# Performance work log

Measured on AMD Instinct MI355X. Metric: run time of the kernel, lower is better.

The kernel has to match this reference:

```python
import jax, jax.numpy as jnp
import numpy as np

BATCH, SEQ, D_IN, D_OUT, RANK = 2, 4096, 4096, 4096, 16


def setup_inputs() -> dict:
    key = jax.random.key(0)
    ks = jax.random.split(key, 5)
    x = jax.random.normal(ks[0], (BATCH, SEQ, D_IN), dtype=jnp.float32)
    W = jax.random.normal(ks[1], (D_OUT, D_IN), dtype=jnp.float32) * 0.02
    bias = jax.random.normal(ks[2], (D_OUT,), dtype=jnp.float32) * 0.02
    A = jax.random.normal(ks[3], (RANK, D_IN), dtype=jnp.float32) * 0.02
    B = jax.random.normal(ks[4], (D_OUT, RANK), dtype=jnp.float32) * 0.02
    return {"x": x, "W": W, "bias": bias, "A": A, "B": B}


def reference(x, W, bias, A, B):
    # base GEMM: F.linear(x, W, bias) -> [b, s, d_out]
    base_out = jnp.einsum("bsi,oi->bso", x, W) + bias
    # LoRA path: einsum('bsi,ri,or->bso', x, A, B), low-rank so contract with A first
    lora_out = jnp.einsum("bsr,or->bso", jnp.einsum("bsi,ri->bsr", x, A), B)
    # original slices lora_out to base_out's last dim; here shapes already match
    return base_out + lora_out[:, :, : base_out.shape[-1]]
```

## Files before the change

kernel.cpp:

```cpp
#include <hip/hip_runtime.h>
#include <hip/hip_bf16.h>


#define M_TOT 8192
#define NDIM  4096
#define KDIM  4096
#define RANK  16

#define BM 128
#define BN 128
#define BK 64

typedef float f4 __attribute__((ext_vector_type(4)));
typedef short s8v __attribute__((ext_vector_type(8)));


static __device__ __forceinline__ unsigned short f2bf(float f) {
  union { float f; unsigned u; } v; v.f = f;
  unsigned r = v.u + 0x7FFF + ((v.u >> 16) & 1);
  return (unsigned short)(r >> 16);
}
static __device__ __forceinline__ unsigned pack2(float lo, float hi) {
  return (unsigned)f2bf(lo) | ((unsigned)f2bf(hi) << 16);
}

static __device__ __forceinline__ void mfma_16x16x32_bf16(f4& d, s8v a, s8v b) {
  asm volatile("v_mfma_f32_16x16x32_bf16 %0, %1, %2, %0"
               : "+v"(d) : "v"(a), "v"(b));
}

#define GLOAD_LDS16(gaddr, laddr)                                              \
  __builtin_amdgcn_global_load_lds(                                            \
      (__attribute__((address_space(1))) void*)(gaddr),                        \
      (__attribute__((address_space(3))) void*)(laddr), 16, 0, 0)


__global__ __launch_bounds__(256) void cast_x_kernel(
    const float* __restrict__ in, unsigned short* __restrict__ out, int n8) {
  int i = blockIdx.x * blockDim.x + threadIdx.x;
  int stride = gridDim.x * blockDim.x;
  for (; i < n8; i += stride) {
    const float4* p = (const float4*)in + (size_t)i * 2;
    float4 a = p[0];
    float4 b = p[1];
    uint4 o;
    o.x = pack2(a.x, a.y);
    o.y = pack2(a.z, a.w);
    o.z = pack2(b.x, b.y);
    o.w = pack2(b.z, b.w);
    ((uint4*)out)[i] = o;
  }
}


__global__ __launch_bounds__(256) void fuse_w_kernel(
    const float* __restrict__ W, const float* __restrict__ A,
    const float* __restrict__ B, unsigned short* __restrict__ Wb) {
  const int t = threadIdx.x;
  const int i = blockIdx.x * 1024 + t * 4;
  const int o0 = blockIdx.y * 64;

  f4 areg[RANK];
#pragma unroll
  for (int r = 0; r < RANK; ++r)
    areg[r] = *(const f4*)(A + (size_t)r * KDIM + i);

  for (int o = o0; o < o0 + 64; ++o) {
    f4 acc = *(const f4*)(W + (size_t)o * KDIM + i);
#pragma unroll
    for (int r = 0; r < RANK; ++r) {
      float br = B[o * RANK + r];
      acc += br * areg[r];
    }
    uint2 pk;
    pk.x = pack2(acc.x, acc.y);
    pk.y = pack2(acc.z, acc.w);
    *(uint2*)(Wb + (size_t)o * KDIM + i) = pk;
  }
}


__global__ __launch_bounds__(256, 2) void gemm_kernel(
    const unsigned short* __restrict__ Xb,
    const unsigned short* __restrict__ Wb,
    const float* __restrict__ bias,
    float* __restrict__ C) {
  __shared__ __attribute__((aligned(16))) unsigned short As[BM * BK];
  __shared__ __attribute__((aligned(16))) unsigned short Bs[BN * BK];

  const int tid  = threadIdx.x;
  const int wave = tid >> 6;
  const int lane = tid & 63;

  const int brow = blockIdx.y * BM;
  const int bcol = blockIdx.x * BN;

  const int srow = wave * 8 + (lane >> 3);
  const int scol = (lane & 7) * 8;

  const unsigned short* gA = Xb + (size_t)(brow + srow) * KDIM + scol;
  const unsigned short* gB = Wb + (size_t)(bcol + srow) * KDIM + scol;
  unsigned short* lA = &As[srow * BK + scol];
  unsigned short* lB = &Bs[srow * BK + scol];

  const int wrow = (wave >> 1) * 64;
  const int wcol = (wave & 1) * 64;
  const int fr = lane & 15;
  const int fq = lane >> 4;

  const unsigned short* rA = &As[(wrow + fr) * BK + fq * 8];
  const unsigned short* rB = &Bs[(wcol + fr) * BK + fq * 8];

  f4 acc[4][4] = {};

  for (int k0 = 0; k0 < KDIM; k0 += BK) {
#pragma unroll
    for (int j = 0; j < 4; ++j)
      GLOAD_LDS16(gA + (size_t)j * 32 * KDIM, lA + j * 32 * BK);
#pragma unroll
    for (int j = 0; j < 4; ++j)
      GLOAD_LDS16(gB + (size_t)j * 32 * KDIM, lB + j * 32 * BK);
    gA += BK;
    gB += BK;
    __syncthreads();

#pragma unroll
    for (int kk = 0; kk < 2; ++kk) {
      s8v af[4], bf[4];
#pragma unroll
      for (int m = 0; m < 4; ++m)
        af[m] = *(const s8v*)(rA + (m * 16) * BK + kk * 32);
#pragma unroll
      for (int n = 0; n < 4; ++n)
        bf[n] = *(const s8v*)(rB + (n * 16) * BK + kk * 32);
#pragma unroll
      for (int m = 0; m < 4; ++m)
#pragma unroll
        for (int n = 0; n < 4; ++n)
          mfma_16x16x32_bf16(acc[m][n], af[m], bf[n]);
    }
    __syncthreads();
  }

#pragma unroll
  for (int n = 0; n < 4; ++n) {
    const int col = bcol + wcol + n * 16 + fr;
    const float bv = bias[col];
#pragma unroll
    for (int m = 0; m < 4; ++m) {
      const int row0 = brow + wrow + m * 16 + fq * 4;
#pragma unroll
      for (int j = 0; j < 4; ++j)
        C[(size_t)(row0 + j) * NDIM + col] = acc[m][n][j] + bv;
    }
  }
}


extern "C" void kernel_launch(void* const* d_in, const int* in_sizes, int n_in,
                              void* d_out, int out_size, void* d_ws, size_t ws_size,
                              hipStream_t stream) {
  const float* x    = (const float*)d_in[0];
  const float* W    = (const float*)d_in[1];
  const float* bias = (const float*)d_in[2];
  const float* A    = (const float*)d_in[3];
  const float* B    = (const float*)d_in[4];
  float* out = (float*)d_out;

  unsigned short* xb = (unsigned short*)d_ws;
  unsigned short* wb = xb + (size_t)M_TOT * KDIM;

  cast_x_kernel<<<2048, 256, 0, stream>>>(x, xb, (M_TOT * KDIM) / 8);
  fuse_w_kernel<<<dim3(KDIM / 1024, NDIM / 64), 256, 0, stream>>>(W, A, B, wb);
  gemm_kernel<<<dim3(NDIM / BN, M_TOT / BM), 256, 0, stream>>>(xb, wb, bias, out);
}
```

Measured before the change: 573.0 us.

## Rewrite GEMM as 256x256 double-buffered, swizzled, 8-wave pipelined kernel

Replaces the 128x128 single-buffered GEMM with a 256x256 tile per 512-thread block. It double-buffers LDS (128KB), XOR-swizzles LDS columns to avoid bank conflicts, and interleaves async global-to-LDS loads for the next tiles with MFMA quarter-steps under barriers and setprio. Workgroup IDs are remapped for L2 locality, and the fuse_w kernel gets more blocks with an unrolled row loop. The aim is to hide memory latency and cut LDS traffic per FLOP, at the cost of higher register and LDS pressure and fragile manual wait counts.

Result: faster. 496.2 us (-13.4%).

```diff
diff --git a/kernel.cpp b/kernel.cpp
--- a/kernel.cpp
+++ b/kernel.cpp
@@ -6,10 +6,6 @@
 #define NDIM  4096
 #define KDIM  4096
 #define RANK  16
-
-#define BM 128
-#define BN 128
-#define BK 64
 
 typedef float f4 __attribute__((ext_vector_type(4)));
 typedef short s8v __attribute__((ext_vector_type(8)));
@@ -58,20 +54,20 @@
     const float* __restrict__ B, unsigned short* __restrict__ Wb) {
   const int t = threadIdx.x;
   const int i = blockIdx.x * 1024 + t * 4;
-  const int o0 = blockIdx.y * 64;
+  const int o0 = blockIdx.y * 8;
 
   f4 areg[RANK];
 #pragma unroll
   for (int r = 0; r < RANK; ++r)
     areg[r] = *(const f4*)(A + (size_t)r * KDIM + i);
 
-  for (int o = o0; o < o0 + 64; ++o) {
+#pragma unroll
+  for (int oo = 0; oo < 8; ++oo) {
+    const int o = o0 + oo;
     f4 acc = *(const f4*)(W + (size_t)o * KDIM + i);
 #pragma unroll
-    for (int r = 0; r < RANK; ++r) {
-      float br = B[o * RANK + r];
-      acc += br * areg[r];
-    }
+    for (int r = 0; r < RANK; ++r)
+      acc += B[o * RANK + r] * areg[r];
     uint2 pk;
     pk.x = pack2(acc.x, acc.y);
     pk.y = pack2(acc.z, acc.w);
@@ -80,78 +76,117 @@
 }
 
 
-__global__ __launch_bounds__(256, 2) void gemm_kernel(
+#define BAR()   __builtin_amdgcn_s_barrier()
+#define WAITL() do { asm volatile("s_waitcnt lgkmcnt(0)" ::: "memory");        \
+                     __builtin_amdgcn_sched_barrier(0); } while (0)
+#define VMC4()  asm volatile("s_waitcnt vmcnt(4)" ::: "memory")
+#define PRIO(x) __builtin_amdgcn_s_setprio(x)
+
+__global__ __launch_bounds__(512, 2) void gemm_kernel(
     const unsigned short* __restrict__ Xb,
     const unsigned short* __restrict__ Wb,
     const float* __restrict__ bias,
     float* __restrict__ C) {
-  __shared__ __attribute__((aligned(16))) unsigned short As[BM * BK];
-  __shared__ __attribute__((aligned(16))) unsigned short Bs[BN * BK];
+  __shared__ __attribute__((aligned(16))) unsigned short lds[65536];
 
   const int tid  = threadIdx.x;
-  const int wave = tid >> 6;
+  const int w    = tid >> 6;
   const int lane = tid & 63;
-
-  const int brow = blockIdx.y * BM;
-  const int bcol = blockIdx.x * BN;
-
-  const int srow = wave * 8 + (lane >> 3);
-  const int scol = (lane & 7) * 8;
-
-  const unsigned short* gA = Xb + (size_t)(brow + srow) * KDIM + scol;
-  const unsigned short* gB = Wb + (size_t)(bcol + srow) * KDIM + scol;
-  unsigned short* lA = &As[srow * BK + scol];
-  unsigned short* lB = &Bs[srow * BK + scol];
-
-  const int wrow = (wave >> 1) * 64;
-  const int wcol = (wave & 1) * 64;
-  const int fr = lane & 15;
-  const int fq = lane >> 4;
-
-  const unsigned short* rA = &As[(wrow + fr) * BK + fq * 8];
-  const unsigned short* rB = &Bs[(wcol + fr) * BK + fq * 8];
-
-  f4 acc[4][4] = {};
-
-  for (int k0 = 0; k0 < KDIM; k0 += BK) {
-#pragma unroll
-    for (int j = 0; j < 4; ++j)
-      GLOAD_LDS16(gA + (size_t)j * 32 * KDIM, lA + j * 32 * BK);
-#pragma unroll
-    for (int j = 0; j < 4; ++j)
-      GLOAD_LDS16(gB + (size_t)j * 32 * KDIM, lB + j * 32 * BK);
-    gA += BK;
-    gB += BK;
-    __syncthreads();
-
-#pragma unroll
-    for (int kk = 0; kk < 2; ++kk) {
-      s8v af[4], bf[4];
-#pragma unroll
-      for (int m = 0; m < 4; ++m)
-        af[m] = *(const s8v*)(rA + (m * 16) * BK + kk * 32);
-#pragma unroll
-      for (int n = 0; n < 4; ++n)
-        bf[n] = *(const s8v*)(rB + (n * 16) * BK + kk * 32);
-#pragma unroll
-      for (int m = 0; m < 4; ++m)
-#pragma unroll
-        for (int n = 0; n < 4; ++n)
-          mfma_16x16x32_bf16(acc[m][n], af[m], bf[n]);
+  const int fr   = lane & 15;
+  const int fq   = lane >> 4;
+
+  const unsigned orig = blockIdx.x;
+  const unsigned wg   = (orig & 7) * 64 + (orig >> 3);
+  const int brow = (int)(wg >> 4) * 256;
+  const int bcol = (int)(wg & 15) * 256;
+
+  const int wrow = (w >> 2) * 128;
+  const int wcol = (w & 3) * 64;
+
+  const int swz = (fr & 7) * 8;
+  const int ck0 = (fq * 8) ^ swz;
+  const int ck1 = (fq * 8 + 32) ^ swz;
+
+  const int srow = (w << 3) + (lane >> 3);
+  const int sdst = (w << 9) + (lane << 3);
+  const int scol = ((lane & 7) ^ (lane >> 3)) << 3;
+  const unsigned short* Xs = Xb + (size_t)(brow + srow) * KDIM + scol;
+  const unsigned short* Ws = Wb + (size_t)(bcol + srow) * KDIM + scol;
+
+  f4 acc[8][4] = {};
+  s8v af[8], bf0[4], bf1[4];
+
+  auto stage = [&](int T, int reg) {
+    const int k0 = (T & 63) << 6;
+    const unsigned short* s =
+        (reg < 2 ? Xs : Ws) + (size_t)(reg & 1) * 128 * KDIM + k0;
+    unsigned short* d = &lds[((T & 1) << 15) + (reg << 13) + sdst];
+    GLOAD_LDS16(s, d);
+    GLOAD_LDS16(s + 64 * KDIM, d + 4096);
+  };
+
+  auto lda = [&](int base, int mh) {
+#pragma unroll
+    for (int mi = 0; mi < 4; ++mi) {
+      const int row = wrow + mh * 64 + mi * 16 + fr;
+      af[mi * 2 + 0] = *(const s8v*)&lds[base + row * 64 + ck0];
+      af[mi * 2 + 1] = *(const s8v*)&lds[base + row * 64 + ck1];
     }
-    __syncthreads();
-  }
-
-#pragma unroll
-  for (int n = 0; n < 4; ++n) {
-    const int col = bcol + wcol + n * 16 + fr;
-    const float bv = bias[col];
-#pragma unroll
-    for (int m = 0; m < 4; ++m) {
-      const int row0 = brow + wrow + m * 16 + fq * 4;
-#pragma unroll
-      for (int j = 0; j < 4; ++j)
-        C[(size_t)(row0 + j) * NDIM + col] = acc[m][n][j] + bv;
+  };
+  auto ldb = [&](s8v* bf, int base, int nh) {
+#pragma unroll
+    for (int ni = 0; ni < 2; ++ni) {
+      const int row = wcol + nh * 32 + ni * 16 + fr;
+      bf[ni * 2 + 0] = *(const s8v*)&lds[base + 16384 + row * 64 + ck0];
+      bf[ni * 2 + 1] = *(const s8v*)&lds[base + 16384 + row * 64 + ck1];
+    }
+  };
+  auto mm = [&](int mh, int nh, const s8v* bf) {
+#pragma unroll
+    for (int kk = 0; kk < 2; ++kk)
+#pragma unroll
+      for (int mi = 0; mi < 4; ++mi)
+#pragma unroll
+        for (int ni = 0; ni < 2; ++ni)
+          mfma_16x16x32_bf16(acc[mh * 4 + mi][nh * 2 + ni],
+                             af[mi * 2 + kk], bf[ni * 2 + kk]);
+  };
+
+  stage(0, 0); stage(0, 2); stage(0, 1); stage(0, 3);
+  stage(1, 2); stage(1, 0);
+  VMC4();
+  BAR();
+
+  for (int t = 0; t < 64; ++t) {
+    const int base = (t & 1) << 15;
+    lda(base, 0); ldb(bf0, base, 0);
+    stage(t + 1, 1);
+    BAR(); WAITL(); PRIO(1); mm(0, 0, bf0); PRIO(0); BAR();
+    ldb(bf1, base, 1);
+    stage(t + 1, 3);
+    BAR(); WAITL(); PRIO(1); mm(0, 1, bf1); PRIO(0); BAR();
+    lda(base, 1);
+    stage(t + 2, 2);
+    BAR(); WAITL(); PRIO(1); mm(1, 1, bf1); PRIO(0); BAR();
+    stage(t + 2, 0);
+    BAR(); WAITL(); PRIO(1); mm(1, 0, bf0); PRIO(0);
+    VMC4();
+    BAR();
+  }
+
+  float bv[4];
+#pragma unroll
+  for (int n = 0; n < 4; ++n) bv[n] = bias[bcol + wcol + n * 16 + fr];
+#pragma unroll
+  for (int m = 0; m < 8; ++m) {
+#pragma unroll
+    for (int jr = 0; jr < 4; ++jr) {
+      const int row = brow + wrow + m * 16 + fq * 4 + jr;
+      float* cp = C + (size_t)row * NDIM + bcol + wcol + fr;
+      cp[0]  = acc[m][0][jr] + bv[0];
+      cp[16] = acc[m][1][jr] + bv[1];
+      cp[32] = acc[m][2][jr] + bv[2];
+      cp[48] = acc[m][3][jr] + bv[3];
     }
   }
 }
@@ -171,6 +206,6 @@
   unsigned short* wb = xb + (size_t)M_TOT * KDIM;
 
   cast_x_kernel<<<2048, 256, 0, stream>>>(x, xb, (M_TOT * KDIM) / 8);
-  fuse_w_kernel<<<dim3(KDIM / 1024, NDIM / 64), 256, 0, stream>>>(W, A, B, wb);
-  gemm_kernel<<<dim3(NDIM / BN, M_TOT / BM), 256, 0, stream>>>(xb, wb, bias, out);
-}
+  fuse_w_kernel<<<dim3(KDIM / 1024, NDIM / 8), 256, 0, stream>>>(W, A, B, wb);
+  gemm_kernel<<<512, 512, 0, stream>>>(xb, wb, bias, out);
+}
```
